# Kernel tuning notes

Hardware: AMD Instinct MI355X
Metric: run time of the kernel (lower is better)

## Reference

```python
import jax, jax.numpy as jnp
import numpy as np

EPS = 1.0 / 137.0  # fine-structure-constant epsilon used throughout the Yat ops


def yat_dense(x, W, b, alpha):
    # x: [..., C], W: [C, F] -> [..., F]
    dot = jnp.einsum('btc,cf->btf', x, W)
    x_norm = jnp.sum(x * x, axis=-1, keepdims=True)        # [..., 1]
    w_norm = jnp.sum(W * W, axis=0)                         # [F]
    dist = x_norm + w_norm - 2.0 * dot
    y = dot * dot / (dist + EPS)
    y = y + b
    F = W.shape[1]
    scale = (np.sqrt(F) / np.log(1.0 + F)) ** 1.0           # base; alpha exponent applied below
    return y * ((np.float32(np.sqrt(F)) / np.float32(np.log1p(F))) ** alpha)


def setup_inputs() -> dict:
    key = jax.random.key(0)
    ks = jax.random.split(key, 8)
    B, T, C = 4, 1024, 768
    x = jax.random.normal(ks[0], (B, T, C), dtype=jnp.float32)
    mask = jnp.tril(jnp.ones((T, T), dtype=bool))[None, None, :, :]  # causal [1,1,T,T]
    sd = 1.0 / np.sqrt(C)
    W_attn = jax.random.normal(ks[1], (C, 3 * C), dtype=jnp.float32) * sd
    b_attn = jnp.zeros((3 * C,), dtype=jnp.float32)
    alpha_attn = jnp.ones((), dtype=jnp.float32)
    W_proj = jax.random.normal(ks[2], (C, C), dtype=jnp.float32) * sd
    b_proj = jnp.zeros((C,), dtype=jnp.float32)
    alpha_proj = jnp.ones((), dtype=jnp.float32)
    return {"x": x, "mask": mask, "W_attn": W_attn, "b_attn": b_attn,
            "alpha_attn": alpha_attn, "W_proj": W_proj, "b_proj": b_proj,
            "alpha_proj": alpha_proj}


def reference(x, mask, W_attn, b_attn, alpha_attn, W_proj, b_proj, alpha_proj):
    B, T, C = x.shape
    H = 12
    D = C // H  # head_dim
    qkv = yat_dense(x, W_attn, b_attn, alpha_attn)          # [B,T,3C]
    qkv = qkv.reshape(B, T, 3 * H, D)
    q, k, v = jnp.array_split(qkv, 3, axis=2)
    q = jnp.transpose(q, (0, 2, 1, 3))                       # [B,H,T,D]
    k = jnp.transpose(k, (0, 2, 1, 3))
    v = jnp.transpose(v, (0, 2, 1, 3))
    scale = 1.0 / np.float32(np.sqrt(D))
    dot = jnp.einsum('bhid,bhjd->bhij', q, k)                # [B,H,T,T]
    sq_dot = jnp.square(dot * scale)
    q_norm = jnp.sum(jnp.square(q), axis=-1)[..., None]      # [B,H,T,1]
    k_norm = jnp.sum(jnp.square(k), axis=-1)[..., None, :]   # [B,H,1,T]
    sq_dist = q_norm + k_norm - 2.0 * dot * scale
    attn = sq_dot / (sq_dist + EPS)
    attn = jnp.where(mask, attn, jnp.finfo(jnp.float32).min)
    attn = jax.nn.softmax(attn, axis=-1)
    out = jnp.einsum('bhij,bhjd->bhid', attn, v)             # [B,H,T,D]
    out = jnp.transpose(out, (0, 2, 1, 3)).reshape(B, T, C)
    out = yat_dense(out, W_proj, b_proj, alpha_proj)         # [B,T,C]
    return out
```

## Files before the change

kernel.cpp:

```cpp
#include <hip/hip_runtime.h>
#include <math.h>

#define EPS_YAT (1.0f/137.0f)

typedef unsigned short u16;
typedef unsigned int u32;
typedef __attribute__((ext_vector_type(8))) __bf16 bf16x8;
typedef __attribute__((ext_vector_type(4))) float f32x4;

__device__ __forceinline__ float4 ld4(const float* p) { return *(const float4*)p; }

__device__ __forceinline__ u16 bf16_rne(float f) {
    u32 u = __float_as_uint(f);
    u32 r = (u + 0x7fffu + ((u >> 16) & 1u)) >> 16;
    return (u16)r;
}
__device__ __forceinline__ float bf16_f(u16 h) {
    return __uint_as_float(((u32)h) << 16);
}

__device__ __forceinline__ void glds16(const u16* g, u16* s) {
    __builtin_amdgcn_global_load_lds(
        (const __attribute__((address_space(1))) void*)g,
        (__attribute__((address_space(3))) void*)s,
        16, 0, 0);
}

__global__ void colnorm_part(const float* __restrict__ W, float* __restrict__ part,
                             int K, int N) {
    __shared__ float sm[256];
    const int col = blockIdx.x * 64 + (threadIdx.x & 63);
    const int q = threadIdx.x >> 6;
    const int rows = K >> 6;
    const int k0 = blockIdx.y * (K >> 4) + q * rows;
    float s = 0.f;
    for (int k = k0; k < k0 + rows; ++k) {
        float w = W[(size_t)k * N + col];
        s += w * w;
    }
    sm[threadIdx.x] = s;
    __syncthreads();
    if (threadIdx.x < 64)
        part[(size_t)blockIdx.y * N + col] =
            sm[threadIdx.x] + sm[threadIdx.x + 64] + sm[threadIdx.x + 128] + sm[threadIdx.x + 192];
}

__global__ void colnorm_reduce(const float* __restrict__ part, float* __restrict__ wn,
                               int N) {
    int gid = blockIdx.x * 256 + threadIdx.x;
    if (gid >= N) return;
    float s = 0.f;
    #pragma unroll
    for (int i = 0; i < 16; ++i) s += part[(size_t)i * N + gid];
    wn[gid] = s;
}

__global__ void rownorm_kernel(const float* __restrict__ X, float* __restrict__ rn, int K) {
    int wave = threadIdx.x >> 6;
    int lane = threadIdx.x & 63;
    int row = blockIdx.x * 4 + wave;
    const float* xr = X + (size_t)row * K;
    float s = 0.f;
    for (int k = lane * 4; k < K; k += 256) {
        float4 v = ld4(xr + k);
        s += v.x * v.x + v.y * v.y + v.z * v.z + v.w * v.w;
    }
    for (int off = 32; off; off >>= 1) s += __shfl_down(s, off);
    if (lane == 0) rn[row] = s;
}

__global__ void rownorm_hl(const u16* __restrict__ Xh, const u16* __restrict__ Xl,
                           float* __restrict__ rn) {
    int wave = threadIdx.x >> 6;
    int lane = threadIdx.x & 63;
    int row = blockIdx.x * 4 + wave;
    const u16* xh = Xh + (size_t)row * 768;
    const u16* xl = Xl + (size_t)row * 768;
    float s = 0.f;
    for (int k = lane * 4; k < 768; k += 256) {
        uint2 hv = *(const uint2*)(xh + k);
        uint2 lv = *(const uint2*)(xl + k);
        float a0 = bf16_f((u16)hv.x)         + bf16_f((u16)lv.x);
        float a1 = bf16_f((u16)(hv.x >> 16)) + bf16_f((u16)(lv.x >> 16));
        float a2 = bf16_f((u16)hv.y)         + bf16_f((u16)lv.y);
        float a3 = bf16_f((u16)(hv.y >> 16)) + bf16_f((u16)(lv.y >> 16));
        s += a0 * a0 + a1 * a1 + a2 * a2 + a3 * a3;
    }
    for (int off = 32; off; off >>= 1) s += __shfl_down(s, off);
    if (lane == 0) rn[row] = s;
}

__global__ void qknorm_kernel(const u16* __restrict__ qh, const u16* __restrict__ ql,
                              float* __restrict__ qn, float* __restrict__ kn) {
    int gid = blockIdx.x * 256 + threadIdx.x;
    int lane = gid & 15;
    int idx = gid >> 4;
    int which = (idx >= 49152) ? 1 : 0;
    int r = idx - which * 49152;
    int t = r & 1023;
    int bh = r >> 10;
    int h = bh % 12, b = bh / 12;
    const size_t off = (size_t)(b * 1024 + t) * 2304 + which * 768 + h * 64 + lane * 4;
    uint2 hv = *(const uint2*)(qh + off);
    uint2 lv = *(const uint2*)(ql + off);
    float a0 = bf16_f((u16)hv.x)         + bf16_f((u16)lv.x);
    float a1 = bf16_f((u16)(hv.x >> 16)) + bf16_f((u16)(lv.x >> 16));
    float a2 = bf16_f((u16)hv.y)         + bf16_f((u16)lv.y);
    float a3 = bf16_f((u16)(hv.y >> 16)) + bf16_f((u16)(lv.y >> 16));
    float s = a0 * a0 + a1 * a1 + a2 * a2 + a3 * a3;
    s += __shfl_xor(s, 1, 16);
    s += __shfl_xor(s, 2, 16);
    s += __shfl_xor(s, 4, 16);
    s += __shfl_xor(s, 8, 16);
    if (lane == 0) (which ? kn : qn)[r] = s;
}

__global__ void split_kernel(const float* __restrict__ X, u16* __restrict__ Xh,
                             u16* __restrict__ Xl, int n4) {
    int gid = blockIdx.x * 256 + threadIdx.x;
    if (gid >= n4) return;
    float4 v = ld4(X + (size_t)gid * 4);
    u16 h0 = bf16_rne(v.x), h1 = bf16_rne(v.y), h2 = bf16_rne(v.z), h3 = bf16_rne(v.w);
    u16 l0 = bf16_rne(v.x - bf16_f(h0));
    u16 l1 = bf16_rne(v.y - bf16_f(h1));
    u16 l2 = bf16_rne(v.z - bf16_f(h2));
    u16 l3 = bf16_rne(v.w - bf16_f(h3));
    uint2 hp, lp;
    hp.x = (u32)h0 | ((u32)h1 << 16); hp.y = (u32)h2 | ((u32)h3 << 16);
    lp.x = (u32)l0 | ((u32)l1 << 16); lp.y = (u32)l2 | ((u32)l3 << 16);
    *(uint2*)(Xh + (size_t)gid * 4) = hp;
    *(uint2*)(Xl + (size_t)gid * 4) = lp;
}

__global__ void split_wt_kernel(const float* __restrict__ W, u16* __restrict__ Th,
                                u16* __restrict__ Tl, int K, int N) {
    __shared__ float tile[64 * 68];
    const int tid = threadIdx.x;
    const int n0 = blockIdx.x << 6;
    const int k0 = blockIdx.y << 6;
    const int rr = tid >> 4;
    const int cc = (tid & 15) << 2;
    #pragma unroll
    for (int s = 0; s < 4; ++s) {
        int k_l = rr + s * 16;
        *(float4*)&tile[k_l * 68 + cc] = ld4(W + (size_t)(k0 + k_l) * N + n0 + cc);
    }
    __syncthreads();
    #pragma unroll
    for (int s = 0; s < 4; ++s) {
        int n_l = rr + s * 16;
        float a0 = tile[(cc + 0) * 68 + n_l];
        float a1 = tile[(cc + 1) * 68 + n_l];
        float a2 = tile[(cc + 2) * 68 + n_l];
        float a3 = tile[(cc + 3) * 68 + n_l];
        u16 h0 = bf16_rne(a0), h1 = bf16_rne(a1), h2 = bf16_rne(a2), h3 = bf16_rne(a3);
        u16 l0 = bf16_rne(a0 - bf16_f(h0));
        u16 l1 = bf16_rne(a1 - bf16_f(h1));
        u16 l2 = bf16_rne(a2 - bf16_f(h2));
        u16 l3 = bf16_rne(a3 - bf16_f(h3));
        uint2 hp, lp;
        hp.x = (u32)h0 | ((u32)h1 << 16); hp.y = (u32)h2 | ((u32)h3 << 16);
        lp.x = (u32)l0 | ((u32)l1 << 16); lp.y = (u32)l2 | ((u32)l3 << 16);
        size_t o = (size_t)(n0 + n_l) * K + k0 + cc;
        *(uint2*)(Th + o) = hp;
        *(uint2*)(Tl + o) = lp;
    }
}

template<int SPLIT>
__global__ __launch_bounds__(256, 2)
void yat_gemm_mfma(const u16* __restrict__ Ah, const u16* __restrict__ Al,
                   const u16* __restrict__ Bh, const u16* __restrict__ Bl,
                   const float* __restrict__ bias, const float* __restrict__ xn,
                   const float* __restrict__ wnc, const float* __restrict__ alphap,
                   const float Fdim, float* __restrict__ out,
                   u16* __restrict__ outh, u16* __restrict__ outl,
                   const int N, const int K) {
    __shared__ __align__(16) u16 lds[2 * 4 * 4096];
    const int tid = threadIdx.x;
    const int m0 = blockIdx.y << 7;
    const int n0 = blockIdx.x << 7;
    const int w = tid >> 6;
    const int l = tid & 63;
    const int wm = (w >> 1) << 6;
    const int wnn = (w & 1) << 6;
    const int lm = l & 15;
    const int kq = l >> 4;

    const int srow = 16 * w + (l >> 2);
    const int scol = (l & 3) << 3;
    const u16* gA1 = Ah + (size_t)(m0 + srow) * K + scol;
    const u16* gA2 = Ah + (size_t)(m0 + 64 + srow) * K + scol;
    const u16* gC1 = Al + (size_t)(m0 + srow) * K + scol;
    const u16* gC2 = Al + (size_t)(m0 + 64 + srow) * K + scol;
    const u16* gB1 = Bh + (size_t)(n0 + srow) * K + scol;
    const u16* gB2 = Bh + (size_t)(n0 + 64 + srow) * K + scol;
    const u16* gD1 = Bl + (size_t)(n0 + srow) * K + scol;
    const u16* gD2 = Bl + (size_t)(n0 + 64 + srow) * K + scol;
    const int wb = w * 512;

    f32x4 acc[4][4] = {};

    #define STAGE(buf, kk) { \
        u16* sb = lds + (buf) * 16384; \
        glds16(gA1 + (kk), sb + wb); \
        glds16(gA2 + (kk), sb + 2048 + wb); \
        glds16(gC1 + (kk), sb + 4096 + wb); \
        glds16(gC2 + (kk), sb + 6144 + wb); \
        glds16(gB1 + (kk), sb + 8192 + wb); \
        glds16(gB2 + (kk), sb + 10240 + wb); \
        glds16(gD1 + (kk), sb + 12288 + wb); \
        glds16(gD2 + (kk), sb + 14336 + wb); }

    STAGE(0, 0);
    __syncthreads();
    int cur = 0;
    for (int k0 = 0; k0 < K; k0 += 32) {
        if (k0 + 32 < K) STAGE(cur ^ 1, k0 + 32);
        const u16* lAh = lds + cur * 16384;
        const u16* lAl = lAh + 4096;
        const u16* lBh = lAh + 8192;
        const u16* lBl = lAh + 12288;

        bf16x8 fah[4], fal[4], fbh[4], fbl[4];
        #pragma unroll
        for (int i = 0; i < 4; ++i) {
            const int ra = (wm + i * 16 + lm) * 32 + kq * 8;
            fah[i] = *(const bf16x8*)&lAh[ra];
            fal[i] = *(const bf16x8*)&lAl[ra];
            const int rb = (wnn + i * 16 + lm) * 32 + kq * 8;
            fbh[i] = *(const bf16x8*)&lBh[rb];
            fbl[i] = *(const bf16x8*)&lBl[rb];
        }
        #pragma unroll
        for (int i = 0; i < 4; ++i)
            #pragma unroll
            for (int j = 0; j < 4; ++j) {
                f32x4 c = acc[i][j];
                c = __builtin_amdgcn_mfma_f32_16x16x32_bf16(fah[i], fbh[j], c, 0, 0, 0);
                c = __builtin_amdgcn_mfma_f32_16x16x32_bf16(fah[i], fbl[j], c, 0, 0, 0);
                c = __builtin_amdgcn_mfma_f32_16x16x32_bf16(fal[i], fbh[j], c, 0, 0, 0);
                acc[i][j] = c;
            }
        __syncthreads();
        cur ^= 1;
    }
    #undef STAGE

    const float scale = powf(sqrtf(Fdim) / log1pf(Fdim), *alphap);
    #pragma unroll
    for (int i = 0; i < 4; ++i) {
        const int mbase = m0 + wm + i * 16 + kq * 4;
        #pragma unroll
        for (int j = 0; j < 4; ++j) {
            const int n = n0 + wnn + j * 16 + lm;
            const float w2 = wnc[n];
            const float bv = bias[n];
            #pragma unroll
            for (int r = 0; r < 4; ++r) {
                const int m = mbase + r;
                float d = acc[i][j][r];
                float den = xn[m] + w2 - 2.f * d + EPS_YAT;
                float v = (d * d / den + bv) * scale;
                if constexpr (SPLIT) {
                    u16 hh = bf16_rne(v);
                    outh[(size_t)m * N + n] = hh;
                    outl[(size_t)m * N + n] = bf16_rne(v - bf16_f(hh));
                } else {
                    out[(size_t)m * N + n] = v;
                }
            }
        }
    }
}

#define MFMA_B16(a, b, c) __builtin_amdgcn_mfma_f32_16x16x32_bf16(a, b, c, 0, 0, 0)

#define ST_TILE(j) { \
    const int kro = ((j)*16 + lm) * 72 + (kq << 3); \
    bf16x8 kh = *(const bf16x8*)&KPh[kro]; \
    bf16x8 kl = *(const bf16x8*)&KPl[kro]; \
    st##j = MFMA_B16(kh, qh0, st##j); \
    st##j = MFMA_B16(kl, qh0, st##j); \
    st##j = MFMA_B16(kh, ql0, st##j); \
    kh = *(const bf16x8*)&KPh[kro + 32]; \
    kl = *(const bf16x8*)&KPl[kro + 32]; \
    st##j = MFMA_B16(kh, qh1, st##j); \
    st##j = MFMA_B16(kl, qh1, st##j); \
    st##j = MFMA_B16(kh, ql1, st##j); \
}

#define YAT_EL(j, r) { \
    float sv = st##j[r] * 0.125f; \
    float den = qnm + kns[(j)*16 + kq4 + (r)] - 2.f * sv + EPS_YAT; \
    float v = sv * sv / den; \
    if (diag && ((j)*16 + kq4 + (r) > wband + lm)) v = -3e38f; \
    st##j[r] = v; mm = fmaxf(mm, v); }
#define YAT_TILE(j) YAT_EL(j,0) YAT_EL(j,1) YAT_EL(j,2) YAT_EL(j,3)

#define PEXP_TILE(j) { \
    float p0 = __expf(st##j[0] - mnew), p1 = __expf(st##j[1] - mnew); \
    float p2 = __expf(st##j[2] - mnew), p3 = __expf(st##j[3] - mnew); \
    rs += p0 + p1 + p2 + p3; \
    u16 h0 = bf16_rne(p0), h1 = bf16_rne(p1), h2 = bf16_rne(p2), h3 = bf16_rne(p3); \
    uint2 hp; hp.x = (u32)h0 | ((u32)h1 << 16); hp.y = (u32)h2 | ((u32)h3 << 16); \
    *(uint2*)&KPh[pmrow + (j)*16 + kq4] = hp; \
    u16 e0 = bf16_rne(p0 - bf16_f(h0)), e1 = bf16_rne(p1 - bf16_f(h1)); \
    u16 e2 = bf16_rne(p2 - bf16_f(h2)), e3 = bf16_rne(p3 - bf16_f(h3)); \
    uint2 lp; lp.x = (u32)e0 | ((u32)e1 << 16); lp.y = (u32)e2 | ((u32)e3 << 16); \
    *(uint2*)&KPl[pmrow + (j)*16 + kq4] = lp; }

#define PV_TILE(j) { \
    const int vro = ((j)*16 + lm) * 72 + vkq8; \
    bf16x8 vh = *(const bf16x8*)&Vth[vro]; \
    bf16x8 vl = *(const bf16x8*)&Vtl[vro]; \
    ac##j = MFMA_B16(ph0, vh, ac##j); \
    ac##j = MFMA_B16(pl0, vh, ac##j); \
    ac##j = MFMA_B16(ph0, vl, ac##j); \
    vh = *(const bf16x8*)&Vth[vro + 32]; \
    vl = *(const bf16x8*)&Vtl[vro + 32]; \
    ac##j = MFMA_B16(ph1, vh, ac##j); \
    ac##j = MFMA_B16(pl1, vh, ac##j); \
    ac##j = MFMA_B16(ph1, vl, ac##j); \
}

#define WRVT(dst, v2, m) { \
    dst[(sj * 4 + 16 * (m) + 0) * 72 + toks] = (u16)((v2).x); \
    dst[(sj * 4 + 16 * (m) + 1) * 72 + toks] = (u16)((v2).x >> 16); \
    dst[(sj * 4 + 16 * (m) + 2) * 72 + toks] = (u16)((v2).y); \
    dst[(sj * 4 + 16 * (m) + 3) * 72 + toks] = (u16)((v2).y >> 16); }

__global__ __launch_bounds__(256, 4)
void yat_flash_mfma(const u16* __restrict__ qh_g, const u16* __restrict__ ql_g,
                    const float* __restrict__ qn, const float* __restrict__ kn,
                    u16* __restrict__ outh, u16* __restrict__ outl) {
    __shared__ __align__(16) u16 KPh[64 * 72], KPl[64 * 72];
    __shared__ __align__(16) u16 Vth[64 * 72], Vtl[64 * 72];
    __shared__ float kns[64];

    const int tid = threadIdx.x;
    const int L = blockIdx.x;
    const int u = L / 48;
    const int qt = (u & 1) ? (u >> 1) : (15 - (u >> 1));
    const int bh = L % 48;
    const int h = bh % 12, b = bh / 12;
    const int wave = tid >> 6;
    const int lane = tid & 63;
    const int lm = lane & 15;
    const int kq = lane >> 4;
    const int kq4 = kq << 2;
    const int wband = wave << 4;
    const int sr = tid >> 2;
    const int sj = tid & 3;
    const int toks = sr ^ (sj << 3);
    const int vkq8 = (kq ^ (lm >> 2)) << 3;
    const size_t base = (size_t)(b * 1024) * 2304 + h * 64;

    {
        const size_t qoff = base + (size_t)((qt << 6) + sr) * 2304 + sj * 16;
        *(uint4*)&KPh[sr * 72 + sj * 16]     = *(const uint4*)(qh_g + qoff);
        *(uint4*)&KPh[sr * 72 + sj * 16 + 8] = *(const uint4*)(qh_g + qoff + 8);
        *(uint4*)&KPl[sr * 72 + sj * 16]     = *(const uint4*)(ql_g + qoff);
        *(uint4*)&KPl[sr * 72 + sj * 16 + 8] = *(const uint4*)(ql_g + qoff + 8);
    }
    const float qnm = qn[bh * 1024 + (qt << 6) + wband + lm];

    const size_t r0 = base + (size_t)sr * 2304;
    uint4 kh0 = *(const uint4*)(qh_g + r0 + 768 + sj * 16);
    uint4 kh1 = *(const uint4*)(qh_g + r0 + 768 + sj * 16 + 8);
    uint4 kl0 = *(const uint4*)(ql_g + r0 + 768 + sj * 16);
    uint4 kl1 = *(const uint4*)(ql_g + r0 + 768 + sj * 16 + 8);
    uint2 vh0 = *(const uint2*)(qh_g + r0 + 1536 + sj * 4);
    uint2 vh1 = *(const uint2*)(qh_g + r0 + 1536 + sj * 4 + 16);
    uint2 vh2 = *(const uint2*)(qh_g + r0 + 1536 + sj * 4 + 32);
    uint2 vh3 = *(const uint2*)(qh_g + r0 + 1536 + sj * 4 + 48);
    uint2 vl0 = *(const uint2*)(ql_g + r0 + 1536 + sj * 4);
    uint2 vl1 = *(const uint2*)(ql_g + r0 + 1536 + sj * 4 + 16);
    uint2 vl2 = *(const uint2*)(ql_g + r0 + 1536 + sj * 4 + 32);
    uint2 vl3 = *(const uint2*)(ql_g + r0 + 1536 + sj * 4 + 48);
    float knS = (tid < 64) ? kn[bh * 1024 + tid] : 0.f;

    __syncthreads();

    const int qrow = (wband + lm) * 72;
    const bf16x8 qh0 = *(const bf16x8*)&KPh[qrow + (kq << 3)];
    const bf16x8 qh1 = *(const bf16x8*)&KPh[qrow + 32 + (kq << 3)];
    const bf16x8 ql0 = *(const bf16x8*)&KPl[qrow + (kq << 3)];
    const bf16x8 ql1 = *(const bf16x8*)&KPl[qrow + 32 + (kq << 3)];

    f32x4 ac0 = {}, ac1 = {}, ac2 = {}, ac3 = {};
    float mrun = -3e38f, lrun = 0.f;
    const int pmrow = (wband + lm) * 72;

    for (int kt = 0; kt <= qt; ++kt) {
        __syncthreads();
        *(uint4*)&KPh[sr * 72 + sj * 16]     = kh0;
        *(uint4*)&KPh[sr * 72 + sj * 16 + 8] = kh1;
        *(uint4*)&KPl[sr * 72 + sj * 16]     = kl0;
        *(uint4*)&KPl[sr * 72 + sj * 16 + 8] = kl1;
        WRVT(Vth, vh0, 0) WRVT(Vth, vh1, 1) WRVT(Vth, vh2, 2) WRVT(Vth, vh3, 3)
        WRVT(Vtl, vl0, 0) WRVT(Vtl, vl1, 1) WRVT(Vtl, vl2, 2) WRVT(Vtl, vl3, 3)
        if (tid < 64) kns[tid] = knS;
        __syncthreads();

        if (kt < qt) {
            const size_t r = base + (size_t)(((kt + 1) << 6) + sr) * 2304;
            kh0 = *(const uint4*)(qh_g + r + 768 + sj * 16);
            kh1 = *(const uint4*)(qh_g + r + 768 + sj * 16 + 8);
            kl0 = *(const uint4*)(ql_g + r + 768 + sj * 16);
            kl1 = *(const uint4*)(ql_g + r + 768 + sj * 16 + 8);
            vh0 = *(const uint2*)(qh_g + r + 1536 + sj * 4);
            vh1 = *(const uint2*)(qh_g + r + 1536 + sj * 4 + 16);
            vh2 = *(const uint2*)(qh_g + r + 1536 + sj * 4 + 32);
            vh3 = *(const uint2*)(qh_g + r + 1536 + sj * 4 + 48);
            vl0 = *(const uint2*)(ql_g + r + 1536 + sj * 4);
            vl1 = *(const uint2*)(ql_g + r + 1536 + sj * 4 + 16);
            vl2 = *(const uint2*)(ql_g + r + 1536 + sj * 4 + 32);
            vl3 = *(const uint2*)(ql_g + r + 1536 + sj * 4 + 48);
            if (tid < 64) knS = kn[bh * 1024 + ((kt + 1) << 6) + tid];
        }

        f32x4 st0 = {}, st1 = {}, st2 = {}, st3 = {};
        __builtin_amdgcn_s_setprio(1);
        ST_TILE(0) ST_TILE(1) ST_TILE(2) ST_TILE(3)
        __builtin_amdgcn_s_setprio(0);
        __syncthreads();

        const bool diag = (kt == qt);
        float mm = -3e38f;
        YAT_TILE(0) YAT_TILE(1) YAT_TILE(2) YAT_TILE(3)
        mm = fmaxf(mm, __shfl_xor(mm, 16));
        mm = fmaxf(mm, __shfl_xor(mm, 32));
        const float mnew = fmaxf(mrun, mm);
        const float al = __expf(mrun - mnew);
        mrun = mnew;
        float rs = 0.f;
        PEXP_TILE(0) PEXP_TILE(1) PEXP_TILE(2) PEXP_TILE(3)
        rs += __shfl_xor(rs, 16);
        rs += __shfl_xor(rs, 32);
        lrun = lrun * al + rs;
        const float a0 = __shfl(al, kq4 + 0, 16);
        const float a1 = __shfl(al, kq4 + 1, 16);
        const float a2 = __shfl(al, kq4 + 2, 16);
        const float a3 = __shfl(al, kq4 + 3, 16);
        ac0[0] *= a0; ac0[1] *= a1; ac0[2] *= a2; ac0[3] *= a3;
        ac1[0] *= a0; ac1[1] *= a1; ac1[2] *= a2; ac1[3] *= a3;
        ac2[0] *= a0; ac2[1] *= a1; ac2[2] *= a2; ac2[3] *= a3;
        ac3[0] *= a0; ac3[1] *= a1; ac3[2] *= a2; ac3[3] *= a3;
        __syncthreads();

        const bf16x8 ph0 = *(const bf16x8*)&KPh[pmrow + (kq << 3)];
        const bf16x8 ph1 = *(const bf16x8*)&KPh[pmrow + 32 + (kq << 3)];
        const bf16x8 pl0 = *(const bf16x8*)&KPl[pmrow + (kq << 3)];
        const bf16x8 pl1 = *(const bf16x8*)&KPl[pmrow + 32 + (kq << 3)];
        __builtin_amdgcn_s_setprio(1);
        PV_TILE(0) PV_TILE(1) PV_TILE(2) PV_TILE(3)
        __builtin_amdgcn_s_setprio(0);
    }

    const float i0 = 1.f / __shfl(lrun, kq4 + 0, 16);
    const float i1 = 1.f / __shfl(lrun, kq4 + 1, 16);
    const float i2 = 1.f / __shfl(lrun, kq4 + 2, 16);
    const float i3 = 1.f / __shfl(lrun, kq4 + 3, 16);
    const size_t obase = (size_t)(b * 1024 + (qt << 6) + wband + kq4) * 768 + h * 64 + lm;
    u16* oph = outh + obase;
    u16* opl = outl + obase;
    #define STORE_E(j, r, iv) { \
        float ov = ac##j[r] * iv; \
        u16 hh = bf16_rne(ov); \
        oph[(size_t)(r) * 768 + (j)*16] = hh; \
        opl[(size_t)(r) * 768 + (j)*16] = bf16_rne(ov - bf16_f(hh)); }
    #define STORE_T(j) { STORE_E(j,0,i0) STORE_E(j,1,i1) STORE_E(j,2,i2) STORE_E(j,3,i3) }
    STORE_T(0) STORE_T(1) STORE_T(2) STORE_T(3)
    #undef STORE_T
    #undef STORE_E
}

extern "C" void kernel_launch(void* const* d_in, const int* in_sizes, int n_in,
                              void* d_out, int out_size, void* d_ws, size_t ws_size,
                              hipStream_t stream) {
    const float* x          = (const float*)d_in[0];
    const float* W_attn     = (const float*)d_in[2];
    const float* b_attn     = (const float*)d_in[3];
    const float* alpha_attn = (const float*)d_in[4];
    const float* W_proj     = (const float*)d_in[5];
    const float* b_proj     = (const float*)d_in[6];
    const float* alpha_proj = (const float*)d_in[7];

    float* ws       = (float*)d_ws;
    u16*   qkvh     = (u16*)ws;
    u16*   qkvl     = (u16*)(ws + 4718592);
    float* xn       = ws + 12582912;
    float* an       = ws + 12587008;
    float* wn_attn  = ws + 12591104;
    float* wn_proj  = ws + 12593408;
    float* qn       = ws + 12594176;
    float* kn       = ws + 12643328;

    float* cn_part_a = ws + 9437184;
    float* cn_part_p = ws + 9437184 + 36864;
    u16* xh  = (u16*)(ws + 9437184);
    u16* xl  = (u16*)(ws + 11010048);
    u16* aoh = (u16*)(ws + 9437184);
    u16* aol = (u16*)(ws + 11010048);
    u16* wth = (u16*)d_out;
    u16* wtl = (u16*)d_out + 1769472;
    u16* wph = (u16*)(ws + 3145728);
    u16* wpl = (u16*)(ws + 3440640);

    colnorm_part<<<dim3(36, 16), 256, 0, stream>>>(W_attn, cn_part_a, 768, 2304);
    colnorm_part<<<dim3(12, 16), 256, 0, stream>>>(W_proj, cn_part_p, 768, 768);
    colnorm_reduce<<<9, 256, 0, stream>>>(cn_part_a, wn_attn, 2304);
    colnorm_reduce<<<3, 256, 0, stream>>>(cn_part_p, wn_proj, 768);
    rownorm_kernel<<<1024, 256, 0, stream>>>(x, xn, 768);
    split_kernel<<<3072, 256, 0, stream>>>(x, xh, xl, 786432);
    split_wt_kernel<<<dim3(36, 12), 256, 0, stream>>>(W_attn, wth, wtl, 768, 2304);
    yat_gemm_mfma<1><<<dim3(18, 32), 256, 0, stream>>>(
        xh, xl, wth, wtl, b_attn, xn, wn_attn, alpha_attn, 2304.f,
        nullptr, qkvh, qkvl, 2304, 768);
    qknorm_kernel<<<6144, 256, 0, stream>>>(qkvh, qkvl, qn, kn);
    yat_flash_mfma<<<768, 256, 0, stream>>>(qkvh, qkvl, qn, kn, aoh, aol);
    rownorm_hl<<<1024, 256, 0, stream>>>(aoh, aol, an);
    split_wt_kernel<<<dim3(12, 12), 256, 0, stream>>>(W_proj, wph, wpl, 768, 768);
    yat_gemm_mfma<0><<<dim3(6, 32), 256, 0, stream>>>(
        aoh, aol, wph, wpl, b_proj, an, wn_proj, alpha_proj, 768.f,
        (float*)d_out, nullptr, nullptr, 768, 768);
}
```

Before: 276.0 us.

## Shrink yat GEMM tiles, drop double buffering, raise occupancy to four blocks

Reworks the split-bf16 MFMA GEMM so each block covers 64 rows and 64*NB columns (128 for the QKV projection, 64 for the output projection) instead of 128x128. The LDS double buffer is replaced by a single buffer with two barriers per K step, and launch bounds rise to four blocks per CU. The goal is more blocks and waves to hide latency and fill the GPU on these small matrices. In exchange, the loss of prefetch overlap exposes load latency inside each block, and the smaller tiles reuse less data.

```diff
diff --git a/kernel.cpp b/kernel.cpp
--- a/kernel.cpp
+++ b/kernel.cpp
@@ -167,8 +167,8 @@
     }
 }
 
-template<int SPLIT>
-__global__ __launch_bounds__(256, 2)
+template<int SPLIT, int NB>
+__global__ __launch_bounds__(256, 4)
 void yat_gemm_mfma(const u16* __restrict__ Ah, const u16* __restrict__ Al,
                    const u16* __restrict__ Bh, const u16* __restrict__ Bl,
                    const float* __restrict__ bias, const float* __restrict__ xn,
@@ -176,84 +176,78 @@
                    const float Fdim, float* __restrict__ out,
                    u16* __restrict__ outh, u16* __restrict__ outl,
                    const int N, const int K) {
-    __shared__ __align__(16) u16 lds[2 * 4 * 4096];
+    __shared__ __align__(16) u16 lds[4096 + NB * 4096];
     const int tid = threadIdx.x;
-    const int m0 = blockIdx.y << 7;
-    const int n0 = blockIdx.x << 7;
+    const int m0 = blockIdx.y << 6;
+    const int n0 = blockIdx.x * (64 * NB);
     const int w = tid >> 6;
     const int l = tid & 63;
-    const int wm = (w >> 1) << 6;
-    const int wnn = (w & 1) << 6;
     const int lm = l & 15;
     const int kq = l >> 4;
-
-    const int srow = 16 * w + (l >> 2);
+    const int kq4 = kq << 2;
+    const int wn = w * 16 * NB;
+
+    const int srow = (w << 4) + (l >> 2);
     const int scol = (l & 3) << 3;
-    const u16* gA1 = Ah + (size_t)(m0 + srow) * K + scol;
-    const u16* gA2 = Ah + (size_t)(m0 + 64 + srow) * K + scol;
-    const u16* gC1 = Al + (size_t)(m0 + srow) * K + scol;
-    const u16* gC2 = Al + (size_t)(m0 + 64 + srow) * K + scol;
-    const u16* gB1 = Bh + (size_t)(n0 + srow) * K + scol;
+    const u16* gA  = Ah + (size_t)(m0 + srow) * K + scol;
+    const u16* gC  = Al + (size_t)(m0 + srow) * K + scol;
+    const u16* gB  = Bh + (size_t)(n0 + srow) * K + scol;
+    const u16* gD  = Bl + (size_t)(n0 + srow) * K + scol;
     const u16* gB2 = Bh + (size_t)(n0 + 64 + srow) * K + scol;
-    const u16* gD1 = Bl + (size_t)(n0 + srow) * K + scol;
     const u16* gD2 = Bl + (size_t)(n0 + 64 + srow) * K + scol;
-    const int wb = w * 512;
-
-    f32x4 acc[4][4] = {};
-
-    #define STAGE(buf, kk) { \
-        u16* sb = lds + (buf) * 16384; \
-        glds16(gA1 + (kk), sb + wb); \
-        glds16(gA2 + (kk), sb + 2048 + wb); \
-        glds16(gC1 + (kk), sb + 4096 + wb); \
-        glds16(gC2 + (kk), sb + 6144 + wb); \
-        glds16(gB1 + (kk), sb + 8192 + wb); \
-        glds16(gB2 + (kk), sb + 10240 + wb); \
-        glds16(gD1 + (kk), sb + 12288 + wb); \
-        glds16(gD2 + (kk), sb + 14336 + wb); }
-
-    STAGE(0, 0);
-    __syncthreads();
-    int cur = 0;
+    const int wb = w << 9;
+
+    u16* sAh = lds;
+    u16* sAl = lds + 2048;
+    u16* sBh = lds + 4096;
+    u16* sBl = lds + 4096 + 2048 * NB;
+
+    f32x4 acc[4][NB] = {};
+
     for (int k0 = 0; k0 < K; k0 += 32) {
-        if (k0 + 32 < K) STAGE(cur ^ 1, k0 + 32);
-        const u16* lAh = lds + cur * 16384;
-        const u16* lAl = lAh + 4096;
-        const u16* lBh = lAh + 8192;
-        const u16* lBl = lAh + 12288;
-
-        bf16x8 fah[4], fal[4], fbh[4], fbl[4];
+        __syncthreads();
+        glds16(gA + k0, sAh + wb);
+        glds16(gC + k0, sAl + wb);
+        glds16(gB + k0, sBh + wb);
+        glds16(gD + k0, sBl + wb);
+        if constexpr (NB == 2) {
+            glds16(gB2 + k0, sBh + 2048 + wb);
+            glds16(gD2 + k0, sBl + 2048 + wb);
+        }
+        __syncthreads();
+
+        bf16x8 fah[4], fal[4], fbh[NB], fbl[NB];
         #pragma unroll
         for (int i = 0; i < 4; ++i) {
-            const int ra = (wm + i * 16 + lm) * 32 + kq * 8;
-            fah[i] = *(const bf16x8*)&lAh[ra];
-            fal[i] = *(const bf16x8*)&lAl[ra];
-            const int rb = (wnn + i * 16 + lm) * 32 + kq * 8;
-            fbh[i] = *(const bf16x8*)&lBh[rb];
-            fbl[i] = *(const bf16x8*)&lBl[rb];
+            const int ra = (i * 16 + lm) * 32 + (kq << 3);
+            fah[i] = *(const bf16x8*)&sAh[ra];
+            fal[i] = *(const bf16x8*)&sAl[ra];
+        }
+        #pragma unroll
+        for (int j = 0; j < NB; ++j) {
+            const int rb = (wn + j * 16 + lm) * 32 + (kq << 3);
+            fbh[j] = *(const bf16x8*)&sBh[rb];
+            fbl[j] = *(const bf16x8*)&sBl[rb];
         }
         #pragma unroll
         for (int i = 0; i < 4; ++i)
             #pragma unroll
-            for (int j = 0; j < 4; ++j) {
+            for (int j = 0; j < NB; ++j) {
                 f32x4 c = acc[i][j];
                 c = __builtin_amdgcn_mfma_f32_16x16x32_bf16(fah[i], fbh[j], c, 0, 0, 0);
                 c = __builtin_amdgcn_mfma_f32_16x16x32_bf16(fah[i], fbl[j], c, 0, 0, 0);
                 c = __builtin_amdgcn_mfma_f32_16x16x32_bf16(fal[i], fbh[j], c, 0, 0, 0);
                 acc[i][j] = c;
             }
-        __syncthreads();
-        cur ^= 1;
-    }
-    #undef STAGE
+    }
 
     const float scale = powf(sqrtf(Fdim) / log1pf(Fdim), *alphap);
     #pragma unroll
     for (int i = 0; i < 4; ++i) {
-        const int mbase = m0 + wm + i * 16 + kq * 4;
+        const int mbase = m0 + i * 16 + kq4;
         #pragma unroll
-        for (int j = 0; j < 4; ++j) {
-            const int n = n0 + wnn + j * 16 + lm;
+        for (int j = 0; j < NB; ++j) {
+            const int n = n0 + wn + j * 16 + lm;
             const float w2 = wnc[n];
             const float bv = bias[n];
             #pragma unroll
@@ -515,14 +509,14 @@
     rownorm_kernel<<<1024, 256, 0, stream>>>(x, xn, 768);
     split_kernel<<<3072, 256, 0, stream>>>(x, xh, xl, 786432);
     split_wt_kernel<<<dim3(36, 12), 256, 0, stream>>>(W_attn, wth, wtl, 768, 2304);
-    yat_gemm_mfma<1><<<dim3(18, 32), 256, 0, stream>>>(
+    yat_gemm_mfma<1, 2><<<dim3(18, 64), 256, 0, stream>>>(
         xh, xl, wth, wtl, b_attn, xn, wn_attn, alpha_attn, 2304.f,
         nullptr, qkvh, qkvl, 2304, 768);
     qknorm_kernel<<<6144, 256, 0, stream>>>(qkvh, qkvl, qn, kn);
     yat_flash_mfma<<<768, 256, 0, stream>>>(qkvh, qkvl, qn, kn, aoh, aol);
     rownorm_hl<<<1024, 256, 0, stream>>>(aoh, aol, an);
     split_wt_kernel<<<dim3(12, 12), 256, 0, stream>>>(W_proj, wph, wpl, 768, 768);
-    yat_gemm_mfma<0><<<dim3(6, 32), 256, 0, stream>>>(
+    yat_gemm_mfma<0, 1><<<dim3(12, 64), 256, 0, stream>>>(
         aoh, aol, wph, wpl, b_proj, an, wn_proj, alpha_proj, 768.f,
         (float*)d_out, nullptr, nullptr, 768, 768);
 }
```

After: 270.6 us. Within noise of the previous version (-1.9%).
